# Optimization experiments

Measured on AMD Instinct MI355X. Metric: run time of the kernel, lower is better.

## Reference

```python
import jax, jax.numpy as jnp
import numpy as np

N, E = 50000, 800000          # nodes, edges
DIN, HEAD, HD = 128, 4, 16    # input dim, heads, per-head dim
DOUT = HEAD * HD              # 64 = head*hd
NEG_SLOPE = 0.01              # torch LeakyReLU default


def _lin(key, fan_in, fan_out):
    # torch nn.Linear default init: U(-1/sqrt(fan_in), 1/sqrt(fan_in))
    kw, kb = jax.random.split(key)
    s = 1.0 / np.sqrt(fan_in)
    W = jax.random.uniform(kw, (fan_in, fan_out), jnp.float32, -s, s)
    b = jax.random.uniform(kb, (fan_out,), jnp.float32, -s, s)
    return W, b


def setup_inputs() -> dict:
    key = jax.random.key(0)
    ks = jax.random.split(key, 8)
    x = jax.random.normal(ks[0], (N, DIN), jnp.float32)
    src = jax.random.randint(ks[1], (E,), 0, N, jnp.int32)
    dst = jax.random.randint(ks[2], (E,), 0, N, jnp.int32)
    Ws, bs = _lin(ks[3], DIN, DOUT)   # relation_aware src linear
    Wd, bd = _lin(ks[4], DIN, DOUT)   # relation_aware dst linear
    Wl, bl = _lin(ks[5], DIN, DOUT)   # w_liner
    Wa, ba = _lin(ks[6], 3 * HD, 1)   # atten
    return dict(x=x, src=src, dst=dst, Ws=Ws, bs=bs, Wd=Wd, bd=bd,
                Wl=Wl, bl=bl, Wa=Wa, ba=ba)


def reference(x, src, dst, Ws, bs, Wd, bd, Wl, bl, Wa, ba):
    # sign_edges: relation-aware per-edge feature edge_sum  [E, DOUT]
    er = jnp.tanh(x[src] @ Ws + bs + (x[dst] @ Wd + bd))

    # w_liner on node features  [N, DOUT]
    h = x @ Wl + bl

    # message: per-edge, per-head concat + linear + leakyrelu score
    sf = h[src].reshape(E, HEAD, HD)
    df = h[dst].reshape(E, HEAD, HD)
    ef = er.reshape(E, HEAD, HD)
    z = jnp.concatenate([sf, df, ef], axis=-1)        # [E, HEAD, 3*HD]
    a = z @ Wa + ba                                    # [E, HEAD, 1]
    a = jnp.where(a >= 0, a, NEG_SLOPE * a)            # leaky relu

    # reduce: mailbox softmax over incoming edges of each dst node
    m = jax.ops.segment_max(a, dst, num_segments=N)    # [N, HEAD, 1]
    m = jnp.where(jnp.isfinite(m), m, 0.0)             # empty mailboxes -> 0
    e = jnp.exp(a - m[dst])
    s = jax.ops.segment_sum(e, dst, num_segments=N)    # [N, HEAD, 1]
    attn = e / jnp.maximum(s[dst], 1e-38)

    out = jax.ops.segment_sum(attn * sf, dst, num_segments=N)
    out = out.reshape(N, DOUT)                         # [N, head*hd]

    # edge_s: mean of edge_sum over incoming edges per node
    deg = jax.ops.segment_sum(jnp.ones((E, 1), x.dtype), dst, num_segments=N)
    edge_s = jax.ops.segment_sum(er, dst, num_segments=N) / jnp.maximum(deg, 1.0)

    return (edge_s, out, h)  # if_sum=False branch: h already [N, head*hd]
```

## Files before the change

kernel.cpp:

```cpp
#include <hip/hip_runtime.h>
#include <math.h>

#define DIN   128
#define DOUT  64
#define NHEAD 4
#define HD    16

typedef __attribute__((ext_vector_type(8))) short bf16x8;
typedef __attribute__((ext_vector_type(8))) unsigned short u16x8;
typedef __attribute__((ext_vector_type(4))) float f32x4;

__device__ __forceinline__ unsigned short f2bf(float f) {
    union { float f; unsigned u; } v; v.f = f;
    unsigned r = v.u + 0x7FFF + ((v.u >> 16) & 1);
    return (unsigned short)(r >> 16);
}
__device__ __forceinline__ float bf2f(unsigned short s) {
    union { unsigned u; float f; } v; v.u = ((unsigned)s) << 16; return v.f;
}

__global__ __launch_bounds__(256)
void k_prep_hist(const float* __restrict__ Ws, const float* __restrict__ Wd,
                 const float* __restrict__ Wl, short* __restrict__ wT,
                 const int* __restrict__ dst, int* __restrict__ degi,
                 int* __restrict__ rank, int E) {
    const int bid = blockIdx.x, tid = threadIdx.x;
    if (bid < 96) {
        const int idx = bid * 256 + tid;
        const int n = idx >> 7, k = idx & 127;
        float v;
        if (n < 64)       v = Ws[k * DOUT + n];
        else if (n < 128) v = Wd[k * DOUT + (n - 64)];
        else              v = Wl[k * DOUT + (n - 128)];
        wT[idx] = (short)f2bf(v);
        return;
    }
    const int e0 = ((bid - 96) * 256 + tid) * 4;
    if (e0 + 3 < E) {
        const int4 d = *(const int4*)&dst[e0];
        int4 r;
        r.x = atomicAdd(&degi[d.x], 1);
        r.y = atomicAdd(&degi[d.y], 1);
        r.z = atomicAdd(&degi[d.z], 1);
        r.w = atomicAdd(&degi[d.w], 1);
        *(int4*)&rank[e0] = r;
    } else {
        for (int e = e0; e < E; ++e) rank[e] = atomicAdd(&degi[dst[e]], 1);
    }
}

__global__ __launch_bounds__(1024)
void k_scan(const int* __restrict__ degi, int* __restrict__ excl,
            int* __restrict__ bsum, int* __restrict__ boff,
            int* __restrict__ total, int* __restrict__ counter, int N, int NB) {
    __shared__ int wsum[16];
    __shared__ int amLast;
    const int tid = threadIdx.x, lane = tid & 63, wid = tid >> 6;
    const int i = blockIdx.x * 1024 + tid;
    int v = (i < N) ? degi[i] : 0;
    int incl = v;
#pragma unroll
    for (int off = 1; off < 64; off <<= 1) {
        int t = __shfl_up(incl, off);
        if (lane >= off) incl += t;
    }
    if (lane == 63) wsum[wid] = incl;
    __syncthreads();
    if (tid < 16) {
        int t = wsum[tid];
#pragma unroll
        for (int off = 1; off < 16; off <<= 1) {
            int u = __shfl_up(t, off);
            if (tid >= off) t += u;
        }
        wsum[tid] = t;
    }
    __syncthreads();
    const int base = (wid > 0) ? wsum[wid - 1] : 0;
    if (i < N) excl[i] = incl - v + base;
    if (tid == 1023) atomicExch(&bsum[blockIdx.x], wsum[15]);
    __syncthreads();
    if (tid == 0) {
        __threadfence();
        amLast = (atomicAdd(counter, 1) == NB - 1) ? 1 : 0;
    }
    __syncthreads();
    if (amLast && tid < 64) {
        int b = (tid < NB) ? atomicAdd(&bsum[tid], 0) : 0;
        int inc = b;
#pragma unroll
        for (int off = 1; off < 64; off <<= 1) {
            int t = __shfl_up(inc, off);
            if (lane >= off) inc += t;
        }
        if (tid < NB) boff[tid] = inc - b;
        if (tid == 63) *total = inc;
    }
}

__global__ __launch_bounds__(64)
void k_node_proj(const float* __restrict__ x, const short* __restrict__ wT,
                 const float* __restrict__ bs, const float* __restrict__ bd,
                 const float* __restrict__ bl, const float* __restrict__ Wa,
                 unsigned short* __restrict__ packed_bf,
                 float* __restrict__ xd,
                 float* __restrict__ alpha_s, float* __restrict__ alpha_d,
                 float* __restrict__ h_out, int N) {
    __shared__ short xs[16 * 136];
    const int lane = threadIdx.x;
    const int lam = lane & 15, g = lane >> 4;
    const int n0 = blockIdx.x * 16;

    {
        const int r = lane >> 2, c0 = (lane & 3) * 32;
        const int nn = n0 + r;
#pragma unroll
        for (int j = 0; j < 8; ++j) {
            float4 v = make_float4(0.f, 0.f, 0.f, 0.f);
            if (nn < N) v = ((const float4*)x)[(size_t)nn * 32 + (c0 >> 2) + j];
            short4 h4;
            h4.x = (short)f2bf(v.x); h4.y = (short)f2bf(v.y);
            h4.z = (short)f2bf(v.z); h4.w = (short)f2bf(v.w);
            *(short4*)&xs[r * 136 + c0 + j * 4] = h4;
        }
    }
    __syncthreads();

    bf16x8 afr[4];
#pragma unroll
    for (int ks = 0; ks < 4; ++ks)
        afr[ks] = *(const bf16x8*)&xs[lam * 136 + ks * 32 + g * 8];

    f32x4 acc[12];
#pragma unroll
    for (int c = 0; c < 12; ++c) acc[c] = (f32x4){0.f, 0.f, 0.f, 0.f};

#pragma unroll
    for (int c = 0; c < 12; ++c) {
#pragma unroll
        for (int ks = 0; ks < 4; ++ks) {
            const bf16x8 b = *(const bf16x8*)&wT[(c * 16 + lam) * 128 + ks * 32 + g * 8];
            acc[c] = __builtin_amdgcn_mfma_f32_16x16x32_bf16(afr[ks], b, acc[c], 0, 0, 0);
        }
    }

    float bsv[4], bdv[4], blv[4];
#pragma unroll
    for (int c = 0; c < 4; ++c) {
        bsv[c] = bs[c * 16 + lam];
        bdv[c] = bd[c * 16 + lam];
        blv[c] = bl[c * 16 + lam];
    }
    const float waS = Wa[lam], waD = Wa[16 + lam];
    const int cc_base = (lam >> 2), t_sl = lam & 3;

#pragma unroll
    for (int i = 0; i < 4; ++i) {
        const int node = n0 + g * 4 + i;
        float xsv[4], xdv[4], hv[4];
#pragma unroll
        for (int c = 0; c < 4; ++c) {
            xsv[c] = acc[c][i]     + bsv[c];
            xdv[c] = acc[4 + c][i] + bdv[c];
            hv[c]  = acc[8 + c][i] + blv[c];
        }
        float p0 = hv[0] * waS, p1 = hv[1] * waS, p2 = hv[2] * waS, p3 = hv[3] * waS;
        float q0 = hv[0] * waD, q1 = hv[1] * waD, q2 = hv[2] * waD, q3 = hv[3] * waD;
#pragma unroll
        for (int off = 1; off < 16; off <<= 1) {
            p0 += __shfl_xor(p0, off); p1 += __shfl_xor(p1, off);
            p2 += __shfl_xor(p2, off); p3 += __shfl_xor(p3, off);
            q0 += __shfl_xor(q0, off); q1 += __shfl_xor(q1, off);
            q2 += __shfl_xor(q2, off); q3 += __shfl_xor(q3, off);
        }
        if (node < N) {
            const size_t rowb = (size_t)node * 128;
#pragma unroll
            for (int c = 0; c < 4; ++c) {
                const int cc = c * 4 + cc_base;
                packed_bf[rowb + cc * 8 + t_sl]     = f2bf(xsv[c]);
                packed_bf[rowb + cc * 8 + 4 + t_sl] = f2bf(hv[c]);
                xd   [(size_t)node * DOUT + c * 16 + lam] = xdv[c];
                h_out[(size_t)node * DOUT + c * 16 + lam] = hv[c];
            }
            if (lam == 0) {
                *(f32x4*)&alpha_s[(size_t)node * NHEAD] = (f32x4){p0, p1, p2, p3};
                *(f32x4*)&alpha_d[(size_t)node * NHEAD] = (f32x4){q0, q1, q2, q3};
            }
        }
    }
}

__global__ __launch_bounds__(256)
void k_scatter(const int* __restrict__ src, const int* __restrict__ dst,
               const int* __restrict__ rp_raw, const int* __restrict__ boff,
               const int* __restrict__ rank, int* __restrict__ srcs_sorted, int E) {
    const int e0 = (blockIdx.x * 256 + threadIdx.x) * 4;
    if (e0 + 3 < E) {
        const int4 s = *(const int4*)&src[e0];
        const int4 d = *(const int4*)&dst[e0];
        const int4 r = *(const int4*)&rank[e0];
        srcs_sorted[rp_raw[d.x] + boff[d.x >> 10] + r.x] = s.x;
        srcs_sorted[rp_raw[d.y] + boff[d.y >> 10] + r.y] = s.y;
        srcs_sorted[rp_raw[d.z] + boff[d.z >> 10] + r.z] = s.z;
        srcs_sorted[rp_raw[d.w] + boff[d.w >> 10] + r.w] = s.w;
    } else {
        for (int e = e0; e < E; ++e) {
            const int d = dst[e];
            srcs_sorted[rp_raw[d] + boff[d >> 10] + rank[e]] = src[e];
        }
    }
}

__global__ __launch_bounds__(256, 8)
void k_aggregate(const int* __restrict__ rp_raw, const int* __restrict__ boff,
                 const int* __restrict__ total, const int* __restrict__ srcs,
                 const unsigned short* __restrict__ packed_bf,
                 const float* __restrict__ xd,
                 const float* __restrict__ alpha_s, const float* __restrict__ alpha_d,
                 const float* __restrict__ Wa, const float* __restrict__ ba,
                 float* __restrict__ edge_s, float* __restrict__ out, int N) {
    const int lane = threadIdx.x & 63;
    const int n = blockIdx.x * 4 + (threadIdx.x >> 6);
    if (n >= N) return;
    const int g = lane >> 4, lam = lane & 15;
    const int hd = lam >> 2, q = lam & 3;

    const int start = rp_raw[n] + boff[n >> 10];
    const int end = (n + 1 < N) ? (rp_raw[n + 1] + boff[(n + 1) >> 10]) : *total;
    const int deg = end - start;
    const int last = end - 1;

    const float4 xd4 = *(const float4*)&xd[(size_t)n * DOUT + lam * 4];
    const float4 wa4 = *(const float4*)&Wa[32 + q * 4];
    const float adb  = alpha_d[n * NHEAD + hd] + ba[0];

    float es0=0.f,es1=0.f,es2=0.f,es3=0.f;
    float o0=0.f,o1=0.f,o2=0.f,o3=0.f;
    float s = 0.f;

    const int niter = (deg + 3) >> 2;
    int e = start + g;

    float vm0=0.f, vm1=0.f, vm2=0.f;
    u16x8 pk0=(u16x8){0,0,0,0,0,0,0,0}, pk1=pk0, pk2=pk0;
    float as0=0.f, as1=0.f, as2=0.f;
    if (niter > 0) {
        {
            vm0 = (e < end) ? 1.f : 0.f;
            const int sn = srcs[min(e, last)];
            pk0 = *(const u16x8*)&packed_bf[(size_t)sn * 128 + lam * 8];
            as0 = alpha_s[sn * NHEAD + hd];
        }
        {
            const int e1 = e + 4;
            vm1 = (e1 < end) ? 1.f : 0.f;
            const int sn = srcs[min(e1, last)];
            pk1 = *(const u16x8*)&packed_bf[(size_t)sn * 128 + lam * 8];
            as1 = alpha_s[sn * NHEAD + hd];
        }
        {
            const int e2 = e + 8;
            vm2 = (e2 < end) ? 1.f : 0.f;
            const int sn = srcs[min(e2, last)];
            pk2 = *(const u16x8*)&packed_bf[(size_t)sn * 128 + lam * 8];
            as2 = alpha_s[sn * NHEAD + hd];
        }
    }

    for (int it = 0; it < niter; ++it) {
        float vmn = 0.f, asn = 0.f;
        u16x8 pkn = (u16x8){0,0,0,0,0,0,0,0};
        const int e3 = e + 12;
        if (it + 3 < niter) {
            vmn = (e3 < end) ? 1.f : 0.f;
            const int sn = srcs[min(e3, last)];
            pkn = *(const u16x8*)&packed_bf[(size_t)sn * 128 + lam * 8];
            asn = alpha_s[sn * NHEAD + hd];
        }

        const float t0 = __expf(2.f * (bf2f(pk0[0]) + xd4.x));
        const float t1 = __expf(2.f * (bf2f(pk0[1]) + xd4.y));
        const float t2 = __expf(2.f * (bf2f(pk0[2]) + xd4.z));
        const float t3 = __expf(2.f * (bf2f(pk0[3]) + xd4.w));
        const float er0 = fmaf(-2.f, __builtin_amdgcn_rcpf(t0 + 1.f), 1.f);
        const float er1 = fmaf(-2.f, __builtin_amdgcn_rcpf(t1 + 1.f), 1.f);
        const float er2 = fmaf(-2.f, __builtin_amdgcn_rcpf(t2 + 1.f), 1.f);
        const float er3 = fmaf(-2.f, __builtin_amdgcn_rcpf(t3 + 1.f), 1.f);
        es0 = fmaf(er0, vm0, es0); es1 = fmaf(er1, vm0, es1);
        es2 = fmaf(er2, vm0, es2); es3 = fmaf(er3, vm0, es3);

        float p = er0 * wa4.x;
        p = fmaf(er1, wa4.y, p);
        p = fmaf(er2, wa4.z, p);
        p = fmaf(er3, wa4.w, p);
        p += __shfl_xor(p, 1);
        p += __shfl_xor(p, 2);

        float a = as0 + adb + p;
        a = (a >= 0.f) ? a : 0.01f * a;
        const float w = __expf(a) * vm0;
        s += w;
        o0 = fmaf(w, bf2f(pk0[4]), o0); o1 = fmaf(w, bf2f(pk0[5]), o1);
        o2 = fmaf(w, bf2f(pk0[6]), o2); o3 = fmaf(w, bf2f(pk0[7]), o3);

        vm0 = vm1; pk0 = pk1; as0 = as1;
        vm1 = vm2; pk1 = pk2; as1 = as2;
        vm2 = vmn; pk2 = pkn; as2 = asn;
        e += 4;
    }

#pragma unroll
    for (int off = 16; off < 64; off <<= 1) {
        es0 += __shfl_xor(es0, off); es1 += __shfl_xor(es1, off);
        es2 += __shfl_xor(es2, off); es3 += __shfl_xor(es3, off);
        o0  += __shfl_xor(o0,  off); o1  += __shfl_xor(o1,  off);
        o2  += __shfl_xor(o2,  off); o3  += __shfl_xor(o3,  off);
        s   += __shfl_xor(s,   off);
    }

    if (g == 0) {
        const float inv_s = __builtin_amdgcn_rcpf(fmaxf(s, 1e-38f));
        const float inv_d = __builtin_amdgcn_rcpf(fmaxf((float)deg, 1.0f));
        const size_t od = (size_t)n * DOUT + lam * 4;
        *(f32x4*)&out[od]    = (f32x4){o0 * inv_s, o1 * inv_s, o2 * inv_s, o3 * inv_s};
        *(f32x4*)&edge_s[od] = (f32x4){es0 * inv_d, es1 * inv_d, es2 * inv_d, es3 * inv_d};
    }
}

extern "C" void kernel_launch(void* const* d_in, const int* in_sizes, int n_in,
                              void* d_out, int out_size, void* d_ws, size_t ws_size,
                              hipStream_t stream) {
    const float* x  = (const float*)d_in[0];
    const int*   src= (const int*)  d_in[1];
    const int*   dst= (const int*)  d_in[2];
    const float* Ws = (const float*)d_in[3];
    const float* bs = (const float*)d_in[4];
    const float* Wd = (const float*)d_in[5];
    const float* bd = (const float*)d_in[6];
    const float* Wl = (const float*)d_in[7];
    const float* bl = (const float*)d_in[8];
    const float* Wa = (const float*)d_in[9];
    const float* ba = (const float*)d_in[10];

    const int N = in_sizes[0] / DIN;
    const int E = in_sizes[1];
    const int NB = (N + 1023) / 1024;

    float* out_f = (float*)d_out;
    float* edge_s_out = out_f;
    float* out_attn   = out_f + (size_t)N * DOUT;
    float* h_out      = out_f + 2 * (size_t)N * DOUT;

    char* ws = (char*)d_ws;
    size_t o = 0;
    unsigned short* packed_bf = (unsigned short*)(ws + o); o += (size_t)N * 128 * 2;
    float* xd      = (float*)(ws + o); o += (size_t)N * DOUT * 4;
    float* alpha_s = (float*)(ws + o); o += (size_t)N * NHEAD * 4;
    float* alpha_d = (float*)(ws + o); o += (size_t)N * NHEAD * 4;
    int*   degi    = (int*)  (ws + o); o += (size_t)N * 4;
    int*   counter = (int*)  (ws + o); o += 64;
    int*   rp_raw  = (int*)  (ws + o); o += (size_t)(N + 1) * 4;
    int*   rank    = (int*)  (ws + o); o += (size_t)E * 4;
    int*   srcs    = (int*)  (ws + o); o += (size_t)E * 4;
    int*   bsum    = (int*)  (ws + o); o += 64 * 4;
    int*   boff    = (int*)  (ws + o); o += 64 * 4;
    int*   total   = (int*)  (ws + o); o += 64;
    short* wT      = (short*)(ws + o); o += (size_t)192 * 128 * 2;

    hipMemsetAsync(degi, 0, (size_t)N * 4 + 64, stream);

    const int HB = (E + 1023) / 1024;
    k_prep_hist<<<96 + HB, 256, 0, stream>>>(Ws, Wd, Wl, wT, dst, degi, rank, E);

    k_scan<<<NB, 1024, 0, stream>>>(degi, rp_raw, bsum, boff, total, counter, N, NB);

    k_node_proj<<<(N + 15) / 16, 64, 0, stream>>>(x, wT, bs, bd, bl, Wa,
                                                  packed_bf, xd, alpha_s, alpha_d,
                                                  h_out, N);

    k_scatter<<<((E + 3) / 4 + 255) / 256, 256, 0, stream>>>(src, dst, rp_raw, boff,
                                                             rank, srcs, E);

    k_aggregate<<<(N + 3) / 4, 256, 0, stream>>>(rp_raw, boff, total, srcs,
                                                 packed_bf, xd,
                                                 alpha_s, alpha_d, Wa, ba,
                                                 edge_s_out, out_attn, N);
}
```

Before: 138.0 us.

## Fuse degree histogram into node projection kernel and unroll aggregate pipeline

Replaces the memset and combined weight-prep/histogram kernel with an init kernel that zeroes degrees and the counter alongside the weight transpose. The edge histogram now runs in the odd blocks of the node projection kernel, interleaved with projection blocks, so the atomic-bound and compute-bound work overlap within one launch. It also unrolls the aggregate loop by three and uses a macro, so the rotation of the prefetch registers is removed. The cost is one more launch slot before scan, a larger grid with idle blocks, and more code in the aggregate kernel that raises register pressure.

```diff
diff --git a/kernel.cpp b/kernel.cpp
--- a/kernel.cpp
+++ b/kernel.cpp
@@ -20,10 +20,9 @@
 }
 
 __global__ __launch_bounds__(256)
-void k_prep_hist(const float* __restrict__ Ws, const float* __restrict__ Wd,
-                 const float* __restrict__ Wl, short* __restrict__ wT,
-                 const int* __restrict__ dst, int* __restrict__ degi,
-                 int* __restrict__ rank, int E) {
+void k_init(const float* __restrict__ Ws, const float* __restrict__ Wd,
+            const float* __restrict__ Wl, short* __restrict__ wT,
+            int* __restrict__ degi, int* __restrict__ counter, int N) {
     const int bid = blockIdx.x, tid = threadIdx.x;
     if (bid < 96) {
         const int idx = bid * 256 + tid;
@@ -33,83 +32,48 @@
         else if (n < 128) v = Wd[k * DOUT + (n - 64)];
         else              v = Wl[k * DOUT + (n - 128)];
         wT[idx] = (short)f2bf(v);
+        if (bid == 0 && tid == 0) *counter = 0;
         return;
     }
-    const int e0 = ((bid - 96) * 256 + tid) * 4;
-    if (e0 + 3 < E) {
-        const int4 d = *(const int4*)&dst[e0];
-        int4 r;
-        r.x = atomicAdd(&degi[d.x], 1);
-        r.y = atomicAdd(&degi[d.y], 1);
-        r.z = atomicAdd(&degi[d.z], 1);
-        r.w = atomicAdd(&degi[d.w], 1);
-        *(int4*)&rank[e0] = r;
-    } else {
-        for (int e = e0; e < E; ++e) rank[e] = atomicAdd(&degi[dst[e]], 1);
-    }
-}
-
-__global__ __launch_bounds__(1024)
-void k_scan(const int* __restrict__ degi, int* __restrict__ excl,
-            int* __restrict__ bsum, int* __restrict__ boff,
-            int* __restrict__ total, int* __restrict__ counter, int N, int NB) {
-    __shared__ int wsum[16];
-    __shared__ int amLast;
-    const int tid = threadIdx.x, lane = tid & 63, wid = tid >> 6;
-    const int i = blockIdx.x * 1024 + tid;
-    int v = (i < N) ? degi[i] : 0;
-    int incl = v;
-#pragma unroll
-    for (int off = 1; off < 64; off <<= 1) {
-        int t = __shfl_up(incl, off);
-        if (lane >= off) incl += t;
-    }
-    if (lane == 63) wsum[wid] = incl;
-    __syncthreads();
-    if (tid < 16) {
-        int t = wsum[tid];
-#pragma unroll
-        for (int off = 1; off < 16; off <<= 1) {
-            int u = __shfl_up(t, off);
-            if (tid >= off) t += u;
-        }
-        wsum[tid] = t;
-    }
-    __syncthreads();
-    const int base = (wid > 0) ? wsum[wid - 1] : 0;
-    if (i < N) excl[i] = incl - v + base;
-    if (tid == 1023) atomicExch(&bsum[blockIdx.x], wsum[15]);
-    __syncthreads();
-    if (tid == 0) {
-        __threadfence();
-        amLast = (atomicAdd(counter, 1) == NB - 1) ? 1 : 0;
-    }
-    __syncthreads();
-    if (amLast && tid < 64) {
-        int b = (tid < NB) ? atomicAdd(&bsum[tid], 0) : 0;
-        int inc = b;
-#pragma unroll
-        for (int off = 1; off < 64; off <<= 1) {
-            int t = __shfl_up(inc, off);
-            if (lane >= off) inc += t;
-        }
-        if (tid < NB) boff[tid] = inc - b;
-        if (tid == 63) *total = inc;
-    }
+    const int i = (bid - 96) * 256 + tid;
+    if (i < N) degi[i] = 0;
 }
 
 __global__ __launch_bounds__(64)
-void k_node_proj(const float* __restrict__ x, const short* __restrict__ wT,
+void k_proj_hist(const float* __restrict__ x, const short* __restrict__ wT,
                  const float* __restrict__ bs, const float* __restrict__ bd,
                  const float* __restrict__ bl, const float* __restrict__ Wa,
                  unsigned short* __restrict__ packed_bf,
-                 float* __restrict__ xd,
-                 float* __restrict__ alpha_s, float* __restrict__ alpha_d,
-                 float* __restrict__ h_out, int N) {
+                 float* __restrict__ xd, float* __restrict__ alpha_s,
+                 float* __restrict__ alpha_d, float* __restrict__ h_out, int N,
+                 const int* __restrict__ dst, int* __restrict__ degi,
+                 int* __restrict__ rank, int E, int NPJ, int NHB) {
     __shared__ short xs[16 * 136];
-    const int lane = threadIdx.x;
+    const int bid = blockIdx.x, tid = threadIdx.x;
+
+    if (bid & 1) {
+        const int hi = bid >> 1;
+        if (hi >= NHB) return;
+        const int e0 = (hi * 64 + tid) * 4;
+        if (e0 + 3 < E) {
+            const int4 d = *(const int4*)&dst[e0];
+            int4 r;
+            r.x = atomicAdd(&degi[d.x], 1);
+            r.y = atomicAdd(&degi[d.y], 1);
+            r.z = atomicAdd(&degi[d.z], 1);
+            r.w = atomicAdd(&degi[d.w], 1);
+            *(int4*)&rank[e0] = r;
+        } else {
+            for (int e = e0; e < E; ++e) rank[e] = atomicAdd(&degi[dst[e]], 1);
+        }
+        return;
+    }
+
+    const int pj = bid >> 1;
+    if (pj >= NPJ) return;
+    const int lane = tid;
     const int lam = lane & 15, g = lane >> 4;
-    const int n0 = blockIdx.x * 16;
+    const int n0 = pj * 16;
 
     {
         const int r = lane >> 2, c0 = (lane & 3) * 32;
@@ -188,6 +152,55 @@
                 *(f32x4*)&alpha_d[(size_t)node * NHEAD] = (f32x4){q0, q1, q2, q3};
             }
         }
+    }
+}
+
+__global__ __launch_bounds__(1024)
+void k_scan(const int* __restrict__ degi, int* __restrict__ excl,
+            int* __restrict__ bsum, int* __restrict__ boff,
+            int* __restrict__ total, int* __restrict__ counter, int N, int NB) {
+    __shared__ int wsum[16];
+    __shared__ int amLast;
+    const int tid = threadIdx.x, lane = tid & 63, wid = tid >> 6;
+    const int i = blockIdx.x * 1024 + tid;
+    int v = (i < N) ? degi[i] : 0;
+    int incl = v;
+#pragma unroll
+    for (int off = 1; off < 64; off <<= 1) {
+        int t = __shfl_up(incl, off);
+        if (lane >= off) incl += t;
+    }
+    if (lane == 63) wsum[wid] = incl;
+    __syncthreads();
+    if (tid < 16) {
+        int t = wsum[tid];
+#pragma unroll
+        for (int off = 1; off < 16; off <<= 1) {
+            int u = __shfl_up(t, off);
+            if (tid >= off) t += u;
+        }
+        wsum[tid] = t;
+    }
+    __syncthreads();
+    const int base = (wid > 0) ? wsum[wid - 1] : 0;
+    if (i < N) excl[i] = incl - v + base;
+    if (tid == 1023) atomicExch(&bsum[blockIdx.x], wsum[15]);
+    __syncthreads();
+    if (tid == 0) {
+        __threadfence();
+        amLast = (atomicAdd(counter, 1) == NB - 1) ? 1 : 0;
+    }
+    __syncthreads();
+    if (amLast && tid < 64) {
+        int b = (tid < NB) ? atomicAdd(&bsum[tid], 0) : 0;
+        int inc = b;
+#pragma unroll
+        for (int off = 1; off < 64; off <<= 1) {
+            int t = __shfl_up(inc, off);
+            if (lane >= off) inc += t;
+        }
+        if (tid < NB) boff[tid] = inc - b;
+        if (tid == 63) *total = inc;
     }
 }
 
@@ -212,6 +225,32 @@
     }
 }
 
+#define AGG_COMPUTE(PK, AS, VM)                                                \
+    {                                                                          \
+        const float t0 = __expf(2.f * (bf2f(PK[0]) + xd4.x));                  \
+        const float t1 = __expf(2.f * (bf2f(PK[1]) + xd4.y));                  \
+        const float t2 = __expf(2.f * (bf2f(PK[2]) + xd4.z));                  \
+        const float t3 = __expf(2.f * (bf2f(PK[3]) + xd4.w));                  \
+        const float er0 = fmaf(-2.f, __builtin_amdgcn_rcpf(t0 + 1.f), 1.f);    \
+        const float er1 = fmaf(-2.f, __builtin_amdgcn_rcpf(t1 + 1.f), 1.f);    \
+        const float er2 = fmaf(-2.f, __builtin_amdgcn_rcpf(t2 + 1.f), 1.f);    \
+        const float er3 = fmaf(-2.f, __builtin_amdgcn_rcpf(t3 + 1.f), 1.f);    \
+        es0 = fmaf(er0, VM, es0); es1 = fmaf(er1, VM, es1);                    \
+        es2 = fmaf(er2, VM, es2); es3 = fmaf(er3, VM, es3);                    \
+        float p = er0 * wa4.x;                                                 \
+        p = fmaf(er1, wa4.y, p);                                               \
+        p = fmaf(er2, wa4.z, p);                                               \
+        p = fmaf(er3, wa4.w, p);                                               \
+        p += __shfl_xor(p, 1);                                                 \
+        p += __shfl_xor(p, 2);                                                 \
+        float a = AS + adb + p;                                                \
+        a = (a >= 0.f) ? a : 0.01f * a;                                        \
+        const float w = __expf(a) * VM;                                        \
+        s += w;                                                                \
+        o0 = fmaf(w, bf2f(PK[4]), o0); o1 = fmaf(w, bf2f(PK[5]), o1);          \
+        o2 = fmaf(w, bf2f(PK[6]), o2); o3 = fmaf(w, bf2f(PK[7]), o3);          \
+    }
+
 __global__ __launch_bounds__(256, 8)
 void k_aggregate(const int* __restrict__ rp_raw, const int* __restrict__ boff,
                  const int* __restrict__ total, const int* __restrict__ srcs,
@@ -240,27 +279,27 @@
     float s = 0.f;
 
     const int niter = (deg + 3) >> 2;
-    int e = start + g;
+    int ebase = start + g;
 
     float vm0=0.f, vm1=0.f, vm2=0.f;
     u16x8 pk0=(u16x8){0,0,0,0,0,0,0,0}, pk1=pk0, pk2=pk0;
     float as0=0.f, as1=0.f, as2=0.f;
     if (niter > 0) {
         {
-            vm0 = (e < end) ? 1.f : 0.f;
-            const int sn = srcs[min(e, last)];
+            vm0 = (ebase < end) ? 1.f : 0.f;
+            const int sn = srcs[min(ebase, last)];
             pk0 = *(const u16x8*)&packed_bf[(size_t)sn * 128 + lam * 8];
             as0 = alpha_s[sn * NHEAD + hd];
         }
         {
-            const int e1 = e + 4;
+            const int e1 = ebase + 4;
             vm1 = (e1 < end) ? 1.f : 0.f;
             const int sn = srcs[min(e1, last)];
             pk1 = *(const u16x8*)&packed_bf[(size_t)sn * 128 + lam * 8];
             as1 = alpha_s[sn * NHEAD + hd];
         }
         {
-            const int e2 = e + 8;
+            const int e2 = ebase + 8;
             vm2 = (e2 < end) ? 1.f : 0.f;
             const int sn = srcs[min(e2, last)];
             pk2 = *(const u16x8*)&packed_bf[(size_t)sn * 128 + lam * 8];
@@ -268,46 +307,54 @@
         }
     }
 
-    for (int it = 0; it < niter; ++it) {
-        float vmn = 0.f, asn = 0.f;
-        u16x8 pkn = (u16x8){0,0,0,0,0,0,0,0};
-        const int e3 = e + 12;
-        if (it + 3 < niter) {
-            vmn = (e3 < end) ? 1.f : 0.f;
-            const int sn = srcs[min(e3, last)];
-            pkn = *(const u16x8*)&packed_bf[(size_t)sn * 128 + lam * 8];
-            asn = alpha_s[sn * NHEAD + hd];
-        }
-
-        const float t0 = __expf(2.f * (bf2f(pk0[0]) + xd4.x));
-        const float t1 = __expf(2.f * (bf2f(pk0[1]) + xd4.y));
-        const float t2 = __expf(2.f * (bf2f(pk0[2]) + xd4.z));
-        const float t3 = __expf(2.f * (bf2f(pk0[3]) + xd4.w));
-        const float er0 = fmaf(-2.f, __builtin_amdgcn_rcpf(t0 + 1.f), 1.f);
-        const float er1 = fmaf(-2.f, __builtin_amdgcn_rcpf(t1 + 1.f), 1.f);
-        const float er2 = fmaf(-2.f, __builtin_amdgcn_rcpf(t2 + 1.f), 1.f);
-        const float er3 = fmaf(-2.f, __builtin_amdgcn_rcpf(t3 + 1.f), 1.f);
-        es0 = fmaf(er0, vm0, es0); es1 = fmaf(er1, vm0, es1);
-        es2 = fmaf(er2, vm0, es2); es3 = fmaf(er3, vm0, es3);
-
-        float p = er0 * wa4.x;
-        p = fmaf(er1, wa4.y, p);
-        p = fmaf(er2, wa4.z, p);
-        p = fmaf(er3, wa4.w, p);
-        p += __shfl_xor(p, 1);
-        p += __shfl_xor(p, 2);
-
-        float a = as0 + adb + p;
-        a = (a >= 0.f) ? a : 0.01f * a;
-        const float w = __expf(a) * vm0;
-        s += w;
-        o0 = fmaf(w, bf2f(pk0[4]), o0); o1 = fmaf(w, bf2f(pk0[5]), o1);
-        o2 = fmaf(w, bf2f(pk0[6]), o2); o3 = fmaf(w, bf2f(pk0[7]), o3);
-
-        vm0 = vm1; pk0 = pk1; as0 = as1;
-        vm1 = vm2; pk1 = pk2; as1 = as2;
-        vm2 = vmn; pk2 = pkn; as2 = asn;
-        e += 4;
+    int it = 0;
+    for (; it + 3 <= niter; it += 3, ebase += 12) {
+        {
+            float vmn = 0.f, asn = 0.f;
+            u16x8 pkn = (u16x8){0,0,0,0,0,0,0,0};
+            const int ep = ebase + 12;
+            if (it + 3 < niter) {
+                vmn = (ep < end) ? 1.f : 0.f;
+                const int sn = srcs[min(ep, last)];
+                pkn = *(const u16x8*)&packed_bf[(size_t)sn * 128 + lam * 8];
+                asn = alpha_s[sn * NHEAD + hd];
+            }
+            AGG_COMPUTE(pk0, as0, vm0);
+            pk0 = pkn; as0 = asn; vm0 = vmn;
+        }
+        {
+            float vmn = 0.f, asn = 0.f;
+            u16x8 pkn = (u16x8){0,0,0,0,0,0,0,0};
+            const int ep = ebase + 16;
+            if (it + 4 < niter) {
+                vmn = (ep < end) ? 1.f : 0.f;
+                const int sn = srcs[min(ep, last)];
+                pkn = *(const u16x8*)&packed_bf[(size_t)sn * 128 + lam * 8];
+                asn = alpha_s[sn * NHEAD + hd];
+            }
+            AGG_COMPUTE(pk1, as1, vm1);
+            pk1 = pkn; as1 = asn; vm1 = vmn;
+        }
+        {
+            float vmn = 0.f, asn = 0.f;
+            u16x8 pkn = (u16x8){0,0,0,0,0,0,0,0};
+            const int ep = ebase + 20;
+            if (it + 5 < niter) {
+                vmn = (ep < end) ? 1.f : 0.f;
+                const int sn = srcs[min(ep, last)];
+                pkn = *(const u16x8*)&packed_bf[(size_t)sn * 128 + lam * 8];
+                asn = alpha_s[sn * NHEAD + hd];
+            }
+            AGG_COMPUTE(pk2, as2, vm2);
+            pk2 = pkn; as2 = asn; vm2 = vmn;
+        }
+    }
+    if (it < niter) {
+        AGG_COMPUTE(pk0, as0, vm0);
+        ++it;
+        if (it < niter) {
+            AGG_COMPUTE(pk1, as1, vm1);
+        }
     }
 
 #pragma unroll
@@ -368,16 +415,16 @@
     int*   total   = (int*)  (ws + o); o += 64;
     short* wT      = (short*)(ws + o); o += (size_t)192 * 128 * 2;
 
-    hipMemsetAsync(degi, 0, (size_t)N * 4 + 64, stream);
-
-    const int HB = (E + 1023) / 1024;
-    k_prep_hist<<<96 + HB, 256, 0, stream>>>(Ws, Wd, Wl, wT, dst, degi, rank, E);
+    k_init<<<96 + (N + 255) / 256, 256, 0, stream>>>(Ws, Wd, Wl, wT, degi, counter, N);
+
+    const int NPJ = (N + 15) / 16;
+    const int NHB = (E + 255) / 256;
+    const int GC  = 2 * ((NPJ > NHB) ? NPJ : NHB);
+    k_proj_hist<<<GC, 64, 0, stream>>>(x, wT, bs, bd, bl, Wa,
+                                       packed_bf, xd, alpha_s, alpha_d, h_out, N,
+                                       dst, degi, rank, E, NPJ, NHB);
 
     k_scan<<<NB, 1024, 0, stream>>>(degi, rp_raw, bsum, boff, total, counter, N, NB);
-
-    k_node_proj<<<(N + 15) / 16, 64, 0, stream>>>(x, wT, bs, bd, bl, Wa,
-                                                  packed_bf, xd, alpha_s, alpha_d,
-                                                  h_out, N);
 
     k_scatter<<<((E + 3) / 4 + 255) / 256, 256, 0, stream>>>(src, dst, rp_raw, boff,
                                                              rank, srcs, E);
```

Result: slower. 204.5 us (+48.2%).

## Fuse degree histogram into node projection kernel via interleaved block roles

Applied to the files above, without the earlier changes.

Replaces the memset plus prep/histogram kernel with an init kernel that converts the weights and zeroes the degree counters. The atomic degree histogram now runs inside the node projection kernel, with odd blocks doing histogram work and even blocks doing projection, so the two overlap in one launch. Intended to remove a launch and a memset and to hide atomic latency behind the projection's compute. The histogram blocks are now 64 threads, which may lower atomic throughput per block, and some blocks exit immediately because the grid is sized to the larger of the two jobs.

```diff
diff --git a/kernel.cpp b/kernel.cpp
--- a/kernel.cpp
+++ b/kernel.cpp
@@ -20,10 +20,9 @@
 }
 
 __global__ __launch_bounds__(256)
-void k_prep_hist(const float* __restrict__ Ws, const float* __restrict__ Wd,
-                 const float* __restrict__ Wl, short* __restrict__ wT,
-                 const int* __restrict__ dst, int* __restrict__ degi,
-                 int* __restrict__ rank, int E) {
+void k_init(const float* __restrict__ Ws, const float* __restrict__ Wd,
+            const float* __restrict__ Wl, short* __restrict__ wT,
+            int* __restrict__ degi, int* __restrict__ counter, int N) {
     const int bid = blockIdx.x, tid = threadIdx.x;
     if (bid < 96) {
         const int idx = bid * 256 + tid;
@@ -33,83 +32,48 @@
         else if (n < 128) v = Wd[k * DOUT + (n - 64)];
         else              v = Wl[k * DOUT + (n - 128)];
         wT[idx] = (short)f2bf(v);
+        if (bid == 0 && tid == 0) *counter = 0;
         return;
     }
-    const int e0 = ((bid - 96) * 256 + tid) * 4;
-    if (e0 + 3 < E) {
-        const int4 d = *(const int4*)&dst[e0];
-        int4 r;
-        r.x = atomicAdd(&degi[d.x], 1);
-        r.y = atomicAdd(&degi[d.y], 1);
-        r.z = atomicAdd(&degi[d.z], 1);
-        r.w = atomicAdd(&degi[d.w], 1);
-        *(int4*)&rank[e0] = r;
-    } else {
-        for (int e = e0; e < E; ++e) rank[e] = atomicAdd(&degi[dst[e]], 1);
-    }
-}
-
-__global__ __launch_bounds__(1024)
-void k_scan(const int* __restrict__ degi, int* __restrict__ excl,
-            int* __restrict__ bsum, int* __restrict__ boff,
-            int* __restrict__ total, int* __restrict__ counter, int N, int NB) {
-    __shared__ int wsum[16];
-    __shared__ int amLast;
-    const int tid = threadIdx.x, lane = tid & 63, wid = tid >> 6;
-    const int i = blockIdx.x * 1024 + tid;
-    int v = (i < N) ? degi[i] : 0;
-    int incl = v;
-#pragma unroll
-    for (int off = 1; off < 64; off <<= 1) {
-        int t = __shfl_up(incl, off);
-        if (lane >= off) incl += t;
-    }
-    if (lane == 63) wsum[wid] = incl;
-    __syncthreads();
-    if (tid < 16) {
-        int t = wsum[tid];
-#pragma unroll
-        for (int off = 1; off < 16; off <<= 1) {
-            int u = __shfl_up(t, off);
-            if (tid >= off) t += u;
-        }
-        wsum[tid] = t;
-    }
-    __syncthreads();
-    const int base = (wid > 0) ? wsum[wid - 1] : 0;
-    if (i < N) excl[i] = incl - v + base;
-    if (tid == 1023) atomicExch(&bsum[blockIdx.x], wsum[15]);
-    __syncthreads();
-    if (tid == 0) {
-        __threadfence();
-        amLast = (atomicAdd(counter, 1) == NB - 1) ? 1 : 0;
-    }
-    __syncthreads();
-    if (amLast && tid < 64) {
-        int b = (tid < NB) ? atomicAdd(&bsum[tid], 0) : 0;
-        int inc = b;
-#pragma unroll
-        for (int off = 1; off < 64; off <<= 1) {
-            int t = __shfl_up(inc, off);
-            if (lane >= off) inc += t;
-        }
-        if (tid < NB) boff[tid] = inc - b;
-        if (tid == 63) *total = inc;
-    }
+    const int i = (bid - 96) * 256 + tid;
+    if (i < N) degi[i] = 0;
 }
 
 __global__ __launch_bounds__(64)
-void k_node_proj(const float* __restrict__ x, const short* __restrict__ wT,
+void k_proj_hist(const float* __restrict__ x, const short* __restrict__ wT,
                  const float* __restrict__ bs, const float* __restrict__ bd,
                  const float* __restrict__ bl, const float* __restrict__ Wa,
                  unsigned short* __restrict__ packed_bf,
-                 float* __restrict__ xd,
-                 float* __restrict__ alpha_s, float* __restrict__ alpha_d,
-                 float* __restrict__ h_out, int N) {
+                 float* __restrict__ xd, float* __restrict__ alpha_s,
+                 float* __restrict__ alpha_d, float* __restrict__ h_out, int N,
+                 const int* __restrict__ dst, int* __restrict__ degi,
+                 int* __restrict__ rank, int E, int NPJ, int NHB) {
     __shared__ short xs[16 * 136];
-    const int lane = threadIdx.x;
+    const int bid = blockIdx.x, tid = threadIdx.x;
+
+    if (bid & 1) {
+        const int hi = bid >> 1;
+        if (hi >= NHB) return;
+        const int e0 = (hi * 64 + tid) * 4;
+        if (e0 + 3 < E) {
+            const int4 d = *(const int4*)&dst[e0];
+            int4 r;
+            r.x = atomicAdd(&degi[d.x], 1);
+            r.y = atomicAdd(&degi[d.y], 1);
+            r.z = atomicAdd(&degi[d.z], 1);
+            r.w = atomicAdd(&degi[d.w], 1);
+            *(int4*)&rank[e0] = r;
+        } else {
+            for (int e = e0; e < E; ++e) rank[e] = atomicAdd(&degi[dst[e]], 1);
+        }
+        return;
+    }
+
+    const int pj = bid >> 1;
+    if (pj >= NPJ) return;
+    const int lane = tid;
     const int lam = lane & 15, g = lane >> 4;
-    const int n0 = blockIdx.x * 16;
+    const int n0 = pj * 16;
 
     {
         const int r = lane >> 2, c0 = (lane & 3) * 32;
@@ -188,6 +152,55 @@
                 *(f32x4*)&alpha_d[(size_t)node * NHEAD] = (f32x4){q0, q1, q2, q3};
             }
         }
+    }
+}
+
+__global__ __launch_bounds__(1024)
+void k_scan(const int* __restrict__ degi, int* __restrict__ excl,
+            int* __restrict__ bsum, int* __restrict__ boff,
+            int* __restrict__ total, int* __restrict__ counter, int N, int NB) {
+    __shared__ int wsum[16];
+    __shared__ int amLast;
+    const int tid = threadIdx.x, lane = tid & 63, wid = tid >> 6;
+    const int i = blockIdx.x * 1024 + tid;
+    int v = (i < N) ? degi[i] : 0;
+    int incl = v;
+#pragma unroll
+    for (int off = 1; off < 64; off <<= 1) {
+        int t = __shfl_up(incl, off);
+        if (lane >= off) incl += t;
+    }
+    if (lane == 63) wsum[wid] = incl;
+    __syncthreads();
+    if (tid < 16) {
+        int t = wsum[tid];
+#pragma unroll
+        for (int off = 1; off < 16; off <<= 1) {
+            int u = __shfl_up(t, off);
+            if (tid >= off) t += u;
+        }
+        wsum[tid] = t;
+    }
+    __syncthreads();
+    const int base = (wid > 0) ? wsum[wid - 1] : 0;
+    if (i < N) excl[i] = incl - v + base;
+    if (tid == 1023) atomicExch(&bsum[blockIdx.x], wsum[15]);
+    __syncthreads();
+    if (tid == 0) {
+        __threadfence();
+        amLast = (atomicAdd(counter, 1) == NB - 1) ? 1 : 0;
+    }
+    __syncthreads();
+    if (amLast && tid < 64) {
+        int b = (tid < NB) ? atomicAdd(&bsum[tid], 0) : 0;
+        int inc = b;
+#pragma unroll
+        for (int off = 1; off < 64; off <<= 1) {
+            int t = __shfl_up(inc, off);
+            if (lane >= off) inc += t;
+        }
+        if (tid < NB) boff[tid] = inc - b;
+        if (tid == 63) *total = inc;
     }
 }
 
@@ -368,16 +381,16 @@
     int*   total   = (int*)  (ws + o); o += 64;
     short* wT      = (short*)(ws + o); o += (size_t)192 * 128 * 2;
 
-    hipMemsetAsync(degi, 0, (size_t)N * 4 + 64, stream);
-
-    const int HB = (E + 1023) / 1024;
-    k_prep_hist<<<96 + HB, 256, 0, stream>>>(Ws, Wd, Wl, wT, dst, degi, rank, E);
+    k_init<<<96 + (N + 255) / 256, 256, 0, stream>>>(Ws, Wd, Wl, wT, degi, counter, N);
+
+    const int NPJ = (N + 15) / 16;
+    const int NHB = (E + 255) / 256;
+    const int GC  = 2 * ((NPJ > NHB) ? NPJ : NHB);
+    k_proj_hist<<<GC, 64, 0, stream>>>(x, wT, bs, bd, bl, Wa,
+                                       packed_bf, xd, alpha_s, alpha_d, h_out, N,
+                                       dst, degi, rank, E, NPJ, NHB);
 
     k_scan<<<NB, 1024, 0, stream>>>(degi, rp_raw, bsum, boff, total, counter, N, NB);
-
-    k_node_proj<<<(N + 15) / 16, 64, 0, stream>>>(x, wT, bs, bd, bl, Wa,
-                                                  packed_bf, xd, alpha_s, alpha_d,
-                                                  h_out, N);
 
     k_scatter<<<((E + 3) / 4 + 255) / 256, 256, 0, stream>>>(src, dst, rp_raw, boff,
                                                              rank, srcs, E);
```

New measurement: 129.9 us. 1.06x faster.
